# Kernel optimization log

Measured on AMD Instinct MI355X. Metric: run time of the kernel, lower is better.

## Reference

```python
import jax, jax.numpy as jnp
import numpy as np

N_NODES = 100000
N_EDGES = 3200000
NUM_FEATURES = 128
HIDDEN = 16


def _gcn_norm(edge_index, num_nodes):
    # Add self-loops and compute symmetric normalization D^{-1/2} (A+I) D^{-1/2}
    loops = jnp.arange(num_nodes, dtype=edge_index.dtype)
    row = jnp.concatenate([edge_index[0], loops])  # source j
    col = jnp.concatenate([edge_index[1], loops])  # target i
    ones = jnp.ones(row.shape[0], dtype=jnp.float32)
    deg = jax.ops.segment_sum(ones, col, num_segments=num_nodes)
    deg_inv_sqrt = jnp.where(deg > 0, jax.lax.rsqrt(deg), 0.0)
    norm = deg_inv_sqrt[row] * deg_inv_sqrt[col]  # [E + N]
    return row, col, norm


def _gcn_conv(x, row, col, norm, W, b, num_nodes):
    h = x @ W                                   # [N, out] linear first (PyG order)
    msg = h[row] * norm[:, None]                # gather + edge-wise scale
    out = jax.ops.segment_sum(msg, col, num_segments=num_nodes)  # scatter-add
    return out + b                              # bias after aggregation (PyG)


def setup_inputs() -> dict:
    key = jax.random.key(0)
    k1, k2, k3, k4, k5 = jax.random.split(key, 5)
    x = jax.random.normal(k1, (N_NODES, NUM_FEATURES), dtype=jnp.float32)
    edge_index = jax.random.randint(k2, (2, N_EDGES), 0, N_NODES, dtype=jnp.int64)
    # Glorot-style init for GCNConv linear weights
    W1 = jax.random.normal(k3, (NUM_FEATURES, HIDDEN), dtype=jnp.float32) / np.sqrt(NUM_FEATURES)
    b1 = jnp.zeros((HIDDEN,), dtype=jnp.float32)
    W2 = jax.random.normal(k4, (HIDDEN, 1), dtype=jnp.float32) / np.sqrt(HIDDEN)
    b2 = jnp.zeros((1,), dtype=jnp.float32)
    return {"x": x, "edge_index": edge_index, "W1": W1, "b1": b1, "W2": W2, "b2": b2}


def reference(x, edge_index, W1, b1, W2, b2):
    num_nodes = x.shape[0]
    row, col, norm = _gcn_norm(edge_index, num_nodes)  # shared by both layers
    h = _gcn_conv(x, row, col, norm, W1, b1, num_nodes)
    h = jax.nn.relu(h)
    out = _gcn_conv(h, row, col, norm, W2, b2, num_nodes)
    return out
```

## Files before the change

kernel.cpp:

```cpp
#include <hip/hip_runtime.h>
#include <hip/hip_fp16.h>


#define CB 8
#define CAP 9216
#define TILE 4096

__global__ void k_init_gcur(int* __restrict__ gcur, int nb) {
    int b = blockIdx.x * blockDim.x + threadIdx.x;
    if (b < nb) gcur[b] = b * CAP;
}

__global__ void __launch_bounds__(512) k_partition(
        const int* __restrict__ row, const int* __restrict__ col,
        int* __restrict__ gcur, int* __restrict__ ebuf, int e, int nb) {
    __shared__ int hist[512];
    __shared__ int lbase[512];
    __shared__ int gdelta[512];
    __shared__ int sval[TILE];
    __shared__ unsigned short sbkt[TILE];
    const int base = blockIdx.x * TILE;
    const int cnt = min(TILE, e - base);
    const int t = threadIdx.x;
    hist[t] = 0;
    __syncthreads();
#pragma unroll
    for (int k = 0; k < TILE / 512; ++k) {
        int i = base + (k << 9) + t;
        if (i < e) atomicAdd(&hist[col[i] >> CB], 1);
    }
    __syncthreads();
    int v = hist[t];
    lbase[t] = v;
    __syncthreads();
    for (int off = 1; off < 512; off <<= 1) {
        int add = (t >= off) ? lbase[t - off] : 0;
        __syncthreads();
        lbase[t] += add;
        __syncthreads();
    }
    int excl = lbase[t] - v;
    __syncthreads();
    lbase[t] = excl;
    int gb = v ? atomicAdd(&gcur[t], v) : 0;
    gdelta[t] = gb - excl;
    hist[t] = excl;
    __syncthreads();
#pragma unroll
    for (int k = 0; k < TILE / 512; ++k) {
        int i = base + (k << 9) + t;
        if (i < e) {
            int c = col[i], r = row[i];
            int b = c >> CB;
            int p = atomicAdd(&hist[b], 1);
            sval[p] = ((c & ((1 << CB) - 1)) << 17) | r;
            sbkt[p] = (unsigned short)b;
        }
    }
    __syncthreads();
    for (int j = t; j < cnt; j += 512) {
        int b = sbkt[j];
        int p = gdelta[b] + j;
        if (p < (b + 1) * CAP) ebuf[p] = sval[j];
    }
}

__global__ void __launch_bounds__(1024) k_bucket(
        const int* __restrict__ ebuf, const int* __restrict__ gcur,
        int* __restrict__ begA, int* __restrict__ endA, int* __restrict__ ssrc,
        float* __restrict__ dis, int n) {
    __shared__ int ev[CAP];
    __shared__ int hist[256];
    __shared__ int sc[256];
    const int b = blockIdx.x, t = threadIdx.x;
    const int base = b * CAP;
    const int cnt = min(gcur[b] - base, CAP);
    if (t < 256) hist[t] = 0;
    __syncthreads();
    for (int j = t; j < cnt; j += 1024) {
        int v = ebuf[base + j];
        ev[j] = v;
        atomicAdd(&hist[v >> 17], 1);
    }
    __syncthreads();
    int v = 0;
    if (t < 256) { v = hist[t]; sc[t] = v; }
    __syncthreads();
    for (int off = 1; off < 256; off <<= 1) {
        int add = 0;
        if (t < 256 && t >= off) add = sc[t - off];
        __syncthreads();
        if (t < 256) sc[t] += add;
        __syncthreads();
    }
    if (t < 256) {
        int excl = sc[t] - v;
        int node = (b << CB) + t;
        if (node < n) {
            begA[node] = base + excl;
            endA[node] = base + excl + v;
            dis[node] = rsqrtf((float)(v + 1));
        }
        hist[t] = excl;
    }
    __syncthreads();
    for (int j = t; j < cnt; j += 1024) {
        int val = ev[j];
        int p = atomicAdd(&hist[val >> 17], 1);
        ssrc[base + p] = val & 0x1FFFF;
    }
}

__global__ void k_gemm1(const float* __restrict__ x, const float* __restrict__ W1,
                        const float* __restrict__ dis, __half* __restrict__ gh, int n) {
    __shared__ float wt[16 * 128];
    for (int t = threadIdx.x; t < 2048; t += blockDim.x) {
        int j = t >> 7, k = t & 127;
        wt[t] = W1[k * 16 + j];
    }
    __syncthreads();
    int t = blockIdx.x * blockDim.x + threadIdx.x;
    if (t >= n * 8) return;
    int r = t >> 3, l = t & 7;
    const float4* x4 = (const float4*)x;
    const float4* w4 = (const float4*)wt;
    float4 va = x4[(size_t)r * 32 + l];
    float4 vb = x4[(size_t)r * 32 + l + 8];
    float4 vc = x4[(size_t)r * 32 + l + 16];
    float4 vd = x4[(size_t)r * 32 + l + 24];
    float acc[16];
#pragma unroll
    for (int j = 0; j < 16; ++j) {
        float4 wa = w4[j * 32 + l];
        float4 wb = w4[j * 32 + l + 8];
        float4 wc = w4[j * 32 + l + 16];
        float4 wd = w4[j * 32 + l + 24];
        acc[j] = va.x * wa.x + va.y * wa.y + va.z * wa.z + va.w * wa.w
               + vb.x * wb.x + vb.y * wb.y + vb.z * wb.z + vb.w * wb.w
               + vc.x * wc.x + vc.y * wc.y + vc.z * wc.z + vc.w * wc.w
               + vd.x * wd.x + vd.y * wd.y + vd.z * wd.z + vd.w * wd.w;
    }
#pragma unroll
    for (int j = 0; j < 16; ++j) {
#pragma unroll
        for (int m = 4; m >= 1; m >>= 1) acc[j] += __shfl_xor(acc[j], m, 8);
    }
    float d = dis[r];
    __half2 hh = __floats2half2_rn(d * acc[2 * l], d * acc[2 * l + 1]);
    ((__half2*)gh)[(size_t)r * 8 + l] = hh;
}

__global__ void k_gather1(const int* __restrict__ begA, const int* __restrict__ endA,
                          const int* __restrict__ ssrc,
                          const __half2* __restrict__ g2, const float* __restrict__ dis,
                          const float* __restrict__ b1, const float* __restrict__ W2,
                          float* __restrict__ tbuf, int n) {
    int t = blockIdx.x * blockDim.x + threadIdx.x;
    if (t >= n * 8) return;
    int i = t >> 3, f2 = t & 7;
    float di = dis[i];
    int beg = begA[i], end = endA[i];
    float2 acc = __half22float2(g2[(size_t)i * 8 + f2]);
    float2 acc1 = make_float2(0.f, 0.f);
    int e = beg;
    for (; e + 8 <= end; e += 8) {
        int s0 = ssrc[e + 0], s1 = ssrc[e + 1], s2 = ssrc[e + 2], s3 = ssrc[e + 3];
        int s4 = ssrc[e + 4], s5 = ssrc[e + 5], s6 = ssrc[e + 6], s7 = ssrc[e + 7];
        float2 v0 = __half22float2(g2[(size_t)s0 * 8 + f2]);
        float2 v1 = __half22float2(g2[(size_t)s1 * 8 + f2]);
        float2 v2 = __half22float2(g2[(size_t)s2 * 8 + f2]);
        float2 v3 = __half22float2(g2[(size_t)s3 * 8 + f2]);
        float2 v4 = __half22float2(g2[(size_t)s4 * 8 + f2]);
        float2 v5 = __half22float2(g2[(size_t)s5 * 8 + f2]);
        float2 v6 = __half22float2(g2[(size_t)s6 * 8 + f2]);
        float2 v7 = __half22float2(g2[(size_t)s7 * 8 + f2]);
        acc.x  += v0.x; acc.y  += v0.y;  acc1.x += v1.x; acc1.y += v1.y;
        acc.x  += v2.x; acc.y  += v2.y;  acc1.x += v3.x; acc1.y += v3.y;
        acc.x  += v4.x; acc.y  += v4.y;  acc1.x += v5.x; acc1.y += v5.y;
        acc.x  += v6.x; acc.y  += v6.y;  acc1.x += v7.x; acc1.y += v7.y;
    }
    for (; e < end; ++e) {
        float2 v = __half22float2(g2[(size_t)ssrc[e] * 8 + f2]);
        acc.x += v.x; acc.y += v.y;
    }
    acc.x += acc1.x; acc.y += acc1.y;
    int f = f2 * 2;
    float u = fmaxf(di * acc.x + b1[f], 0.f) * W2[f]
            + fmaxf(di * acc.y + b1[f + 1], 0.f) * W2[f + 1];
#pragma unroll
    for (int m = 4; m >= 1; m >>= 1) u += __shfl_xor(u, m, 8);
    if (f2 == 0) tbuf[i] = di * u;
}

__global__ void k_gather2(const int* __restrict__ begA, const int* __restrict__ endA,
                          const int* __restrict__ ssrc,
                          const float* __restrict__ tbuf, const float* __restrict__ dis,
                          const float* __restrict__ b2, float* __restrict__ out, int n) {
    int t = blockIdx.x * blockDim.x + threadIdx.x;
    if (t >= n * 8) return;
    int i = t >> 3, l = t & 7;
    int beg = begA[i], end = endA[i];
    float acc = (l == 0) ? tbuf[i] : 0.f;
    float acc1 = 0.f;
    int e = beg + l;
    for (; e + 24 < end; e += 32) {
        int s0 = ssrc[e], s1 = ssrc[e + 8], s2 = ssrc[e + 16], s3 = ssrc[e + 24];
        float v0 = tbuf[s0], v1 = tbuf[s1], v2 = tbuf[s2], v3 = tbuf[s3];
        acc += v0; acc1 += v1; acc += v2; acc1 += v3;
    }
    for (; e < end; e += 8) acc += tbuf[ssrc[e]];
    acc += acc1;
#pragma unroll
    for (int m = 4; m >= 1; m >>= 1) acc += __shfl_xor(acc, m, 8);
    if (l == 0) out[i] = dis[i] * acc + b2[0];
}

extern "C" void kernel_launch(void* const* d_in, const int* in_sizes, int n_in,
                              void* d_out, int out_size, void* d_ws, size_t ws_size,
                              hipStream_t stream) {
    const float* x  = (const float*)d_in[0];
    const int*   ei = (const int*)d_in[1];
    const float* W1 = (const float*)d_in[2];
    const float* b1 = (const float*)d_in[3];
    const float* W2 = (const float*)d_in[4];
    const float* b2 = (const float*)d_in[5];
    float* out = (float*)d_out;

    const int N = in_sizes[0] / 128;
    const int E = in_sizes[1] / 2;
    const int* row = ei;
    const int* col = ei + E;
    const int NB = (N + 255) >> CB;
    const size_t PADE = (size_t)NB * CAP;

    size_t bigsz = PADE > (size_t)N * 8 ? PADE : (size_t)N * 8;
    int*    ebuf = (int*)d_ws;
    __half* gh   = (__half*)d_ws;
    int*    ssrc = (int*)d_ws + bigsz;
    float*  dis  = (float*)(ssrc + PADE);
    float*  tbuf = dis + N;
    int*    begA = (int*)(tbuf + N);
    int*    endA = begA + N;
    int*    gcur = endA + N;

    auto cdiv = [](int a, int b) { return (a + b - 1) / b; };

    k_init_gcur<<<cdiv(NB, 256),    256,  0, stream>>>(gcur, NB);
    k_partition<<<cdiv(E, TILE),    512,  0, stream>>>(row, col, gcur, ebuf, E, NB);
    k_bucket   <<<NB,               1024, 0, stream>>>(ebuf, gcur, begA, endA, ssrc, dis, N);
    k_gemm1    <<<cdiv(N * 8, 256), 256,  0, stream>>>(x, W1, dis, gh, N);
    k_gather1  <<<cdiv(N * 8, 256), 256,  0, stream>>>(begA, endA, ssrc, (const __half2*)gh,
                                                       dis, b1, W2, tbuf, N);
    k_gather2  <<<cdiv(N * 8, 256), 256,  0, stream>>>(begA, endA, ssrc, tbuf, dis, b2, out, N);
}
```

Baseline: 210.1 us.

## Fuse bucket sort with first-layer gather; split degree computation into separate kernel

Replaces the bucket-sort kernel with a light degree-histogram kernel that only produces dis for the GEMM, then fuses the per-bucket counting sort with the layer-1 neighbor gather. The sorted source indices stay in LDS for the gather instead of being re-read from global memory, and the workspace no longer aliases ebuf with gh. It also drops a redundant barrier and store in the partition kernel. In exchange, ebuf is now read twice, the fused kernel uses very large LDS (about 74KB per block), and it runs only NB (~391) blocks of 1024 threads for the gather, which may limit latency hiding.

```diff
diff --git a/kernel.cpp b/kernel.cpp
--- a/kernel.cpp
+++ b/kernel.cpp
@@ -40,8 +40,6 @@
         __syncthreads();
     }
     int excl = lbase[t] - v;
-    __syncthreads();
-    lbase[t] = excl;
     int gb = v ? atomicAdd(&gcur[t], v) : 0;
     gdelta[t] = gb - excl;
     hist[t] = excl;
@@ -65,49 +63,23 @@
     }
 }
 
-__global__ void __launch_bounds__(1024) k_bucket(
+__global__ void __launch_bounds__(256) k_deg(
         const int* __restrict__ ebuf, const int* __restrict__ gcur,
-        int* __restrict__ begA, int* __restrict__ endA, int* __restrict__ ssrc,
         float* __restrict__ dis, int n) {
-    __shared__ int ev[CAP];
-    __shared__ int hist[256];
-    __shared__ int sc[256];
+    __shared__ int h4[4][256];
     const int b = blockIdx.x, t = threadIdx.x;
     const int base = b * CAP;
     const int cnt = min(gcur[b] - base, CAP);
-    if (t < 256) hist[t] = 0;
-    __syncthreads();
-    for (int j = t; j < cnt; j += 1024) {
-        int v = ebuf[base + j];
-        ev[j] = v;
-        atomicAdd(&hist[v >> 17], 1);
-    }
-    __syncthreads();
-    int v = 0;
-    if (t < 256) { v = hist[t]; sc[t] = v; }
-    __syncthreads();
-    for (int off = 1; off < 256; off <<= 1) {
-        int add = 0;
-        if (t < 256 && t >= off) add = sc[t - off];
-        __syncthreads();
-        if (t < 256) sc[t] += add;
-        __syncthreads();
-    }
-    if (t < 256) {
-        int excl = sc[t] - v;
-        int node = (b << CB) + t;
-        if (node < n) {
-            begA[node] = base + excl;
-            endA[node] = base + excl + v;
-            dis[node] = rsqrtf((float)(v + 1));
-        }
-        hist[t] = excl;
-    }
-    __syncthreads();
-    for (int j = t; j < cnt; j += 1024) {
-        int val = ev[j];
-        int p = atomicAdd(&hist[val >> 17], 1);
-        ssrc[base + p] = val & 0x1FFFF;
+    const int sub = (t >> 6) & 3;
+#pragma unroll
+    for (int s = 0; s < 4; ++s) h4[s][t] = 0;
+    __syncthreads();
+    for (int j = t; j < cnt; j += 256) atomicAdd(&h4[sub][ebuf[base + j] >> 17], 1);
+    __syncthreads();
+    int node = (b << CB) + t;
+    if (node < n) {
+        int v = h4[0][t] + h4[1][t] + h4[2][t] + h4[3][t];
+        dis[node] = rsqrtf((float)(v + 1));
     }
 }
 
@@ -150,46 +122,103 @@
     ((__half2*)gh)[(size_t)r * 8 + l] = hh;
 }
 
-__global__ void k_gather1(const int* __restrict__ begA, const int* __restrict__ endA,
-                          const int* __restrict__ ssrc,
-                          const __half2* __restrict__ g2, const float* __restrict__ dis,
-                          const float* __restrict__ b1, const float* __restrict__ W2,
-                          float* __restrict__ tbuf, int n) {
-    int t = blockIdx.x * blockDim.x + threadIdx.x;
-    if (t >= n * 8) return;
-    int i = t >> 3, f2 = t & 7;
-    float di = dis[i];
-    int beg = begA[i], end = endA[i];
-    float2 acc = __half22float2(g2[(size_t)i * 8 + f2]);
-    float2 acc1 = make_float2(0.f, 0.f);
+__global__ void __launch_bounds__(1024) k_fused1(
+        const int* __restrict__ ebuf, const int* __restrict__ gcur,
+        const __half2* __restrict__ g2, const float* __restrict__ b1,
+        const float* __restrict__ W2, int* __restrict__ begA,
+        int* __restrict__ endA, int* __restrict__ ssrc,
+        float* __restrict__ tbuf, int n) {
+    __shared__ int ev[CAP];
+    __shared__ int srt[CAP];
+    __shared__ int hist[256];
+    __shared__ int sc[256];
+    __shared__ int begL[256];
+    __shared__ int cntL[256];
+    __shared__ float sdis[256];
+    __shared__ float sB[16], sW[16];
+    const int b = blockIdx.x, t = threadIdx.x;
+    const int base = b * CAP;
+    const int cnt = min(gcur[b] - base, CAP);
+    if (t < 256) hist[t] = 0;
+    if (t >= 256 && t < 272) { sB[t - 256] = b1[t - 256]; sW[t - 256] = W2[t - 256]; }
+    __syncthreads();
+    for (int j = t; j < cnt; j += 1024) {
+        int v = ebuf[base + j];
+        ev[j] = v;
+        atomicAdd(&hist[v >> 17], 1);
+    }
+    __syncthreads();
+    int v = 0;
+    if (t < 256) { v = hist[t]; sc[t] = v; }
+    __syncthreads();
+    for (int off = 1; off < 256; off <<= 1) {
+        int add = 0;
+        if (t < 256 && t >= off) add = sc[t - off];
+        __syncthreads();
+        if (t < 256) sc[t] += add;
+        __syncthreads();
+    }
+    if (t < 256) {
+        int excl = sc[t] - v;
+        begL[t] = excl;
+        cntL[t] = v;
+        sdis[t] = rsqrtf((float)(v + 1));
+        int node = (b << CB) + t;
+        if (node < n) {
+            begA[node] = base + excl;
+            endA[node] = base + excl + v;
+        }
+        hist[t] = excl;
+    }
+    __syncthreads();
+    for (int j = t; j < cnt; j += 1024) {
+        int val = ev[j];
+        int p = atomicAdd(&hist[val >> 17], 1);
+        int s = val & 0x1FFFF;
+        srt[p] = s;
+        ssrc[base + p] = s;
+    }
+    __syncthreads();
+    int node = t >> 2, l = t & 3;
+    int gnode = (b << CB) + node;
+    if (gnode >= n) return;
+    float di = sdis[node];
+    int beg = begL[node], end = beg + cntL[node];
+    int k0 = l * 2, k1 = l * 2 + 1;
+    float2 acc0 = __half22float2(g2[(size_t)gnode * 8 + k0]);
+    float2 acc1 = __half22float2(g2[(size_t)gnode * 8 + k1]);
+    float2 bcc0 = make_float2(0.f, 0.f), bcc1 = make_float2(0.f, 0.f);
     int e = beg;
-    for (; e + 8 <= end; e += 8) {
-        int s0 = ssrc[e + 0], s1 = ssrc[e + 1], s2 = ssrc[e + 2], s3 = ssrc[e + 3];
-        int s4 = ssrc[e + 4], s5 = ssrc[e + 5], s6 = ssrc[e + 6], s7 = ssrc[e + 7];
-        float2 v0 = __half22float2(g2[(size_t)s0 * 8 + f2]);
-        float2 v1 = __half22float2(g2[(size_t)s1 * 8 + f2]);
-        float2 v2 = __half22float2(g2[(size_t)s2 * 8 + f2]);
-        float2 v3 = __half22float2(g2[(size_t)s3 * 8 + f2]);
-        float2 v4 = __half22float2(g2[(size_t)s4 * 8 + f2]);
-        float2 v5 = __half22float2(g2[(size_t)s5 * 8 + f2]);
-        float2 v6 = __half22float2(g2[(size_t)s6 * 8 + f2]);
-        float2 v7 = __half22float2(g2[(size_t)s7 * 8 + f2]);
-        acc.x  += v0.x; acc.y  += v0.y;  acc1.x += v1.x; acc1.y += v1.y;
-        acc.x  += v2.x; acc.y  += v2.y;  acc1.x += v3.x; acc1.y += v3.y;
-        acc.x  += v4.x; acc.y  += v4.y;  acc1.x += v5.x; acc1.y += v5.y;
-        acc.x  += v6.x; acc.y  += v6.y;  acc1.x += v7.x; acc1.y += v7.y;
+    for (; e + 4 <= end; e += 4) {
+        int s0 = srt[e], s1 = srt[e + 1], s2 = srt[e + 2], s3 = srt[e + 3];
+        float2 a0 = __half22float2(g2[(size_t)s0 * 8 + k0]);
+        float2 a1 = __half22float2(g2[(size_t)s0 * 8 + k1]);
+        float2 b0 = __half22float2(g2[(size_t)s1 * 8 + k0]);
+        float2 b1v = __half22float2(g2[(size_t)s1 * 8 + k1]);
+        float2 c0 = __half22float2(g2[(size_t)s2 * 8 + k0]);
+        float2 c1 = __half22float2(g2[(size_t)s2 * 8 + k1]);
+        float2 d0 = __half22float2(g2[(size_t)s3 * 8 + k0]);
+        float2 d1 = __half22float2(g2[(size_t)s3 * 8 + k1]);
+        acc0.x += a0.x; acc0.y += a0.y; acc1.x += a1.x; acc1.y += a1.y;
+        bcc0.x += b0.x; bcc0.y += b0.y; bcc1.x += b1v.x; bcc1.y += b1v.y;
+        acc0.x += c0.x; acc0.y += c0.y; acc1.x += c1.x; acc1.y += c1.y;
+        bcc0.x += d0.x; bcc0.y += d0.y; bcc1.x += d1.x; bcc1.y += d1.y;
     }
     for (; e < end; ++e) {
-        float2 v = __half22float2(g2[(size_t)ssrc[e] * 8 + f2]);
-        acc.x += v.x; acc.y += v.y;
-    }
-    acc.x += acc1.x; acc.y += acc1.y;
-    int f = f2 * 2;
-    float u = fmaxf(di * acc.x + b1[f], 0.f) * W2[f]
-            + fmaxf(di * acc.y + b1[f + 1], 0.f) * W2[f + 1];
-#pragma unroll
-    for (int m = 4; m >= 1; m >>= 1) u += __shfl_xor(u, m, 8);
-    if (f2 == 0) tbuf[i] = di * u;
+        int s = srt[e];
+        float2 a0 = __half22float2(g2[(size_t)s * 8 + k0]);
+        float2 a1 = __half22float2(g2[(size_t)s * 8 + k1]);
+        acc0.x += a0.x; acc0.y += a0.y; acc1.x += a1.x; acc1.y += a1.y;
+    }
+    acc0.x += bcc0.x; acc0.y += bcc0.y; acc1.x += bcc1.x; acc1.y += bcc1.y;
+    int f = l * 4;
+    float u = fmaxf(di * acc0.x + sB[f], 0.f) * sW[f]
+            + fmaxf(di * acc0.y + sB[f + 1], 0.f) * sW[f + 1]
+            + fmaxf(di * acc1.x + sB[f + 2], 0.f) * sW[f + 2]
+            + fmaxf(di * acc1.y + sB[f + 3], 0.f) * sW[f + 3];
+    u += __shfl_xor(u, 1, 4);
+    u += __shfl_xor(u, 2, 4);
+    if (l == 0) tbuf[gnode] = di * u;
 }
 
 __global__ void k_gather2(const int* __restrict__ begA, const int* __restrict__ endA,
@@ -233,10 +262,9 @@
     const int NB = (N + 255) >> CB;
     const size_t PADE = (size_t)NB * CAP;
 
-    size_t bigsz = PADE > (size_t)N * 8 ? PADE : (size_t)N * 8;
     int*    ebuf = (int*)d_ws;
-    __half* gh   = (__half*)d_ws;
-    int*    ssrc = (int*)d_ws + bigsz;
+    __half* gh   = (__half*)((int*)d_ws + PADE);
+    int*    ssrc = (int*)d_ws + PADE + (size_t)N * 8;
     float*  dis  = (float*)(ssrc + PADE);
     float*  tbuf = dis + N;
     int*    begA = (int*)(tbuf + N);
@@ -247,9 +275,9 @@
 
     k_init_gcur<<<cdiv(NB, 256),    256,  0, stream>>>(gcur, NB);
     k_partition<<<cdiv(E, TILE),    512,  0, stream>>>(row, col, gcur, ebuf, E, NB);
-    k_bucket   <<<NB,               1024, 0, stream>>>(ebuf, gcur, begA, endA, ssrc, dis, N);
+    k_deg      <<<NB,               256,  0, stream>>>(ebuf, gcur, dis, N);
     k_gemm1    <<<cdiv(N * 8, 256), 256,  0, stream>>>(x, W1, dis, gh, N);
-    k_gather1  <<<cdiv(N * 8, 256), 256,  0, stream>>>(begA, endA, ssrc, (const __half2*)gh,
-                                                       dis, b1, W2, tbuf, N);
+    k_fused1   <<<NB,               1024, 0, stream>>>(ebuf, gcur, (const __half2*)gh,
+                                                       b1, W2, begA, endA, ssrc, tbuf, N);
     k_gather2  <<<cdiv(N * 8, 256), 256,  0, stream>>>(begA, endA, ssrc, tbuf, dis, b2, out, N);
 }
```

New measurement: 214.5 us. 2.1% more time.
